# Optimization experiments

Hardware: AMD Instinct MI355X
Metric: run time of the kernel (lower is better)

## Reference

```python
import jax, jax.numpy as jnp
import numpy as np

B, IN_DIM, OUT_DIM = 4096, 2048, 2048
EMA_M = 0.95
LN_EPS = 1e-5


def setup_inputs() -> dict:
    key = jax.random.key(0)
    ks = jax.random.split(key, 8)
    x = jax.random.normal(ks[0], (B, IN_DIM), dtype=jnp.float32)
    # W_slow is orthogonal-init in torch (gain 0.5); scaled gaussian is a fine stand-in for math testing
    W_slow = jax.random.normal(ks[1], (OUT_DIM, IN_DIM), dtype=jnp.float32) * (0.5 / np.sqrt(IN_DIM))
    # buffers start at zero in torch; use small nonzero values so the medium/fast GEMMs are exercised
    W_medium = jax.random.normal(ks[2], (OUT_DIM, IN_DIM), dtype=jnp.float32) * 0.01
    W_fast = jax.random.normal(ks[3], (OUT_DIM, IN_DIM), dtype=jnp.float32) * 0.01
    ln_gamma = jnp.ones((OUT_DIM,), jnp.float32) + 0.1 * jax.random.normal(ks[4], (OUT_DIM,), dtype=jnp.float32)
    ln_beta = 0.1 * jax.random.normal(ks[5], (OUT_DIM,), dtype=jnp.float32)
    pc_w1 = jax.random.normal(ks[6], (8, 3), dtype=jnp.float32) * 0.5
    pc_b1 = jnp.zeros((8,), jnp.float32)
    pc_w2 = jax.random.normal(ks[7], (1, 8), dtype=jnp.float32) * 0.5
    pc_b2 = jnp.full((1,), -1.5, jnp.float32)  # torch fills last Linear bias with -1.5
    ema_mean = jnp.zeros((1,), jnp.float32)
    ema_std = jnp.ones((1,), jnp.float32)
    return {"x": x, "W_slow": W_slow, "W_medium": W_medium, "W_fast": W_fast,
            "ln_gamma": ln_gamma, "ln_beta": ln_beta,
            "pc_w1": pc_w1, "pc_b1": pc_b1, "pc_w2": pc_w2, "pc_b2": pc_b2,
            "ema_mean": ema_mean, "ema_std": ema_std}


def reference(x, W_slow, W_medium, W_fast, ln_gamma, ln_beta,
              pc_w1, pc_b1, pc_w2, pc_b2, ema_mean, ema_std):
    xc = jnp.clip(x, -5.0, 5.0)
    slow_out = jnp.clip(xc @ W_slow.T, -10.0, 10.0)
    pre_act = jnp.clip(slow_out + xc @ W_medium.T + xc @ W_fast.T, -10.0, 10.0)  # [B, OUT]

    batch_mean = pre_act.mean(axis=1, keepdims=True)                      # [B,1]
    batch_std = jnp.maximum(pre_act.std(axis=1, keepdims=True), 1e-6)     # [B,1], ddof=0

    # EMA buffer update (no-grad in torch); clamps applied after update
    new_mean = jnp.clip(EMA_M * ema_mean + (1.0 - EMA_M) * batch_mean.mean(), -0.5, 0.5)
    new_std = jnp.clip(EMA_M * ema_std + (1.0 - EMA_M) * batch_std.mean(), 0.1, 1.5)
    homeostasis = new_std / (jnp.abs(new_mean) + 1e-6)                    # [1]

    stats = jnp.concatenate([batch_mean, batch_std,
                             jnp.broadcast_to(homeostasis[None, :], (batch_mean.shape[0], 1))], axis=1)  # [B,3]
    h = jax.nn.gelu(stats @ pc_w1.T + pc_b1, approximate=False)           # torch GELU is exact erf
    learned_plasticity = jax.nn.sigmoid(h @ pc_w2.T + pc_b2)[:, 0]        # [B] (does not affect `out`)
    _ = learned_plasticity  # kept for fidelity with original compute graph

    # LayerNorm over last dim, eps=1e-5
    mu = pre_act.mean(axis=-1, keepdims=True)
    var = pre_act.var(axis=-1, keepdims=True)
    normed = (pre_act - mu) * jax.lax.rsqrt(var + LN_EPS) * ln_gamma + ln_beta
    out = 5.0 * jnp.tanh(normed / 5.0)
    return out
```

## Files before the change

### kernel.cpp

```cpp
#include <hip/hip_runtime.h>
#include <hip/hip_bf16.h>

#define BDIM    4096
#define IN_DIM  2048
#define OUT_DIM 2048

typedef __attribute__((ext_vector_type(4))) float  floatx4;
typedef __attribute__((ext_vector_type(8))) short  bf16x8;

__device__ __forceinline__ unsigned short f2bf(float f) {
    union { float f; unsigned u; } v; v.f = f;
    unsigned r = v.u + 0x7FFFu + ((v.u >> 16) & 1u);
    return (unsigned short)(r >> 16);
}

__device__ __forceinline__ float bf2f(unsigned short h) {
    union { unsigned u; float f; } v; v.u = (unsigned)h << 16;
    return v.f;
}

__device__ __forceinline__ void async16(const unsigned short* g, unsigned short* l) {
    __builtin_amdgcn_global_load_lds(
        (const __attribute__((address_space(1))) unsigned int*)g,
        (__attribute__((address_space(3))) unsigned int*)l,
        16, 0, 0);
}

__global__ __launch_bounds__(256) void prep(const float* __restrict__ x,
                                            const float* __restrict__ Ws,
                                            const float* __restrict__ Wm,
                                            const float* __restrict__ Wf,
                                            unsigned short* __restrict__ xc,
                                            unsigned short* __restrict__ bsum) {
    int b = blockIdx.x;
    if (b < 8192) {
        int i = b * 256 + threadIdx.x;
        float4 v = ((const float4*)x)[i];
        ushort4 o;
        o.x = f2bf(fminf(fmaxf(v.x, -5.f), 5.f));
        o.y = f2bf(fminf(fmaxf(v.y, -5.f), 5.f));
        o.z = f2bf(fminf(fmaxf(v.z, -5.f), 5.f));
        o.w = f2bf(fminf(fmaxf(v.w, -5.f), 5.f));
        ((ushort4*)xc)[i] = o;
    } else {
        int i = (b - 8192) * 256 + threadIdx.x;
        float4 s = ((const float4*)Ws)[i];
        float4 m = ((const float4*)Wm)[i];
        float4 f = ((const float4*)Wf)[i];
        ushort4 o;
        o.x = f2bf(s.x + m.x + f.x);
        o.y = f2bf(s.y + m.y + f.y);
        o.z = f2bf(s.z + m.z + f.z);
        o.w = f2bf(s.w + m.w + f.w);
        ((ushort4*)bsum)[i] = o;
    }
}

#define TILE   128
#define BK     64
#define KSPLIT 2
#define KHALF  (IN_DIM / KSPLIT)
#define ITERS  (KHALF / BK)

#define MEMBAR() asm volatile("" ::: "memory")

__global__ __launch_bounds__(256, 3) void gemm_bt(const unsigned short* __restrict__ A,
                                                  const unsigned short* __restrict__ B,
                                                  unsigned short* __restrict__ Cpart) {
    constexpr int N = OUT_DIM, K = IN_DIM;
    __shared__ __align__(16) unsigned short As[2 * TILE * BK];
    __shared__ __align__(16) unsigned short Bs[TILE * BK];

    const int tid  = threadIdx.x;
    const int lane = tid & 63;
    const int wave = tid >> 6;
    const int wm   = (wave >> 1) * 64;
    const int wn   = (wave & 1) * 64;
    const int rowBlock = blockIdx.y * TILE;
    const int colBlock = blockIdx.x * TILE;
    const int kBase    = blockIdx.z * KHALF;
    unsigned short* C = Cpart + (size_t)blockIdx.z * BDIM * OUT_DIM;

    const int sRow = tid >> 3;
    const int sSeg = (tid & 7) ^ (sRow & 7);
    const unsigned short* aSrc = A + (size_t)(rowBlock + sRow) * K + kBase + sSeg * 8;
    const unsigned short* bSrc = B + (size_t)(colBlock + sRow) * K + kBase + sSeg * 8;

    floatx4 acc[4][4] = {};

    const int fragRow = lane & 15;
    const int quad    = lane >> 4;
    const int l7      = lane & 7;

    auto stageA = [&](int t, int p) {
        unsigned short* ad = As + p * TILE * BK + tid * 8;
        const unsigned short* ag = aSrc + t * BK;
#pragma unroll
        for (int r = 0; r < 4; r++)
            async16(ag + (size_t)(r * 32) * K, ad + r * 32 * BK);
    };
    auto stageB = [&](int t) {
        unsigned short* bd = Bs + tid * 8;
        const unsigned short* bg = bSrc + t * BK;
#pragma unroll
        for (int r = 0; r < 4; r++)
            async16(bg + (size_t)(r * 32) * K, bd + r * 32 * BK);
    };

    stageB(0);
    stageA(0, 0);
    stageA(1, 1);
    __builtin_amdgcn_s_waitcnt(0xF74);
    MEMBAR();
    __builtin_amdgcn_s_barrier();
    MEMBAR();

    for (int k = 0; k < ITERS; k++) {
        const unsigned short* Ab = As + (k & 1) * TILE * BK;

#pragma unroll
        for (int kk = 0; kk < 2; kk++) {
            const int xs = ((quad + kk * 4) ^ l7) << 3;
            bf16x8 af[4], bfr[4];
#pragma unroll
            for (int i = 0; i < 4; i++) {
                af[i]  = *(const bf16x8*)(Ab + (wm + i * 16 + fragRow) * BK + xs);
                bfr[i] = *(const bf16x8*)(Bs + (wn + i * 16 + fragRow) * BK + xs);
            }
#pragma unroll
            for (int i = 0; i < 4; i++)
#pragma unroll
                for (int j = 0; j < 4; j++)
                    acc[i][j] = __builtin_amdgcn_mfma_f32_16x16x32_bf16(af[i], bfr[j], acc[i][j], 0, 0, 0);
        }

        if (k == ITERS - 1) break;
        MEMBAR();
        __builtin_amdgcn_s_barrier();
        MEMBAR();
        stageB(k + 1);
        if (k + 2 < ITERS) {
            stageA(k + 2, k & 1);
            __builtin_amdgcn_s_waitcnt(0xF74);
        } else {
            __builtin_amdgcn_s_waitcnt(0xF70);
        }
        MEMBAR();
        __builtin_amdgcn_s_barrier();
        MEMBAR();
    }

    const int cCol = colBlock + wn + (lane & 15);
    const int cRow = rowBlock + wm + quad * 4;
#pragma unroll
    for (int i = 0; i < 4; i++) {
#pragma unroll
        for (int j = 0; j < 4; j++) {
            const int col = cCol + j * 16;
            const int rb  = cRow + i * 16;
#pragma unroll
            for (int r = 0; r < 4; r++)
                C[(size_t)(rb + r) * N + col] = f2bf(acc[i][j][r]);
        }
    }
}

__global__ __launch_bounds__(256) void ln_kernel(const unsigned short* __restrict__ Cpart,
                                                 const float* __restrict__ gamma,
                                                 const float* __restrict__ beta,
                                                 float* __restrict__ out) {
    const int row = blockIdx.x;
    const int tid = threadIdx.x;
    __shared__ float wsum[4], wsq[4];

    const uint2* Ca = (const uint2*)(Cpart + (size_t)row * OUT_DIM);
    const uint2* Cb = (const uint2*)(Cpart + (size_t)BDIM * OUT_DIM + (size_t)row * OUT_DIM);

    float4 p[2];
    float sum = 0.f, sq = 0.f;
#pragma unroll
    for (int it = 0; it < 2; it++) {
        uint2 ua = Ca[tid + it * 256];
        uint2 ub = Cb[tid + it * 256];
        float4 q;
        q.x = bf2f((unsigned short)(ua.x & 0xFFFF)) + bf2f((unsigned short)(ub.x & 0xFFFF));
        q.y = bf2f((unsigned short)(ua.x >> 16))    + bf2f((unsigned short)(ub.x >> 16));
        q.z = bf2f((unsigned short)(ua.y & 0xFFFF)) + bf2f((unsigned short)(ub.y & 0xFFFF));
        q.w = bf2f((unsigned short)(ua.y >> 16))    + bf2f((unsigned short)(ub.y >> 16));
        q.x = fminf(fmaxf(q.x, -10.f), 10.f);
        q.y = fminf(fmaxf(q.y, -10.f), 10.f);
        q.z = fminf(fmaxf(q.z, -10.f), 10.f);
        q.w = fminf(fmaxf(q.w, -10.f), 10.f);
        p[it] = q;
        sum += q.x + q.y + q.z + q.w;
        sq  += q.x * q.x + q.y * q.y + q.z * q.z + q.w * q.w;
    }
#pragma unroll
    for (int off = 32; off > 0; off >>= 1) {
        sum += __shfl_down(sum, off);
        sq  += __shfl_down(sq,  off);
    }
    if ((tid & 63) == 0) { wsum[tid >> 6] = sum; wsq[tid >> 6] = sq; }
    __syncthreads();
    const float tsum = wsum[0] + wsum[1] + wsum[2] + wsum[3];
    const float tsq  = wsq[0]  + wsq[1]  + wsq[2]  + wsq[3];
    const float mu   = tsum * (1.0f / OUT_DIM);
    const float var  = tsq * (1.0f / OUT_DIM) - mu * mu;
    const float inv  = rsqrtf(var + 1e-5f);

#pragma unroll
    for (int it = 0; it < 2; it++) {
        int i = tid + it * 256;
        float4 q = p[it];
        float4 g = *(const float4*)(gamma + i * 4);
        float4 b = *(const float4*)(beta + i * 4);
        float4 o;
        float zx = (q.x - mu) * inv * g.x + b.x;
        float zy = (q.y - mu) * inv * g.y + b.y;
        float zz = (q.z - mu) * inv * g.z + b.z;
        float zw = (q.w - mu) * inv * g.w + b.w;
        o.x = 5.f * (1.f - 2.f / (__expf(0.4f * zx) + 1.f));
        o.y = 5.f * (1.f - 2.f / (__expf(0.4f * zy) + 1.f));
        o.z = 5.f * (1.f - 2.f / (__expf(0.4f * zz) + 1.f));
        o.w = 5.f * (1.f - 2.f / (__expf(0.4f * zw) + 1.f));
        *(float4*)(out + (size_t)row * OUT_DIM + i * 4) = o;
    }
}

extern "C" void kernel_launch(void* const* d_in, const int* in_sizes, int n_in,
                              void* d_out, int out_size, void* d_ws, size_t ws_size,
                              hipStream_t stream) {
    const float* x     = (const float*)d_in[0];
    const float* Ws    = (const float*)d_in[1];
    const float* Wm    = (const float*)d_in[2];
    const float* Wf    = (const float*)d_in[3];
    const float* gamma = (const float*)d_in[4];
    const float* beta  = (const float*)d_in[5];
    float* out = (float*)d_out;

    char* ws = (char*)d_ws;
    unsigned short* xc   = (unsigned short*)ws;
    unsigned short* bsum = (unsigned short*)(ws + (size_t)16 * 1024 * 1024);
    unsigned short* Cbuf = (unsigned short*)(ws + (size_t)24 * 1024 * 1024);

    prep<<<12288, 256, 0, stream>>>(x, Ws, Wm, Wf, xc, bsum);
    dim3 g(OUT_DIM / TILE, BDIM / TILE, KSPLIT);
    gemm_bt<<<g, 256, 0, stream>>>(xc, bsum, Cbuf);
    ln_kernel<<<BDIM, 256, 0, stream>>>(Cbuf, gamma, beta, out);
}
```

Baseline: 185.3 us.

## Load B fragments directly from global into registers, drop B LDS staging

Removes the shared-memory staging buffer for the B (weight) tile. Each wave now loads its MFMA B fragments straight from global memory into registers, double-buffered across the two k-halves and prefetched one iteration ahead. This cuts LDS footprint and LDS read/write traffic, which may allow higher occupancy. In exchange each wave issues redundant, less coalesced global loads (16-byte chunks strided across rows), and the waitcnt values are retuned to match the new count of outstanding loads.

```diff
diff --git a/kernel.cpp b/kernel.cpp
--- a/kernel.cpp
+++ b/kernel.cpp
@@ -69,7 +69,6 @@
                                                   unsigned short* __restrict__ Cpart) {
     constexpr int N = OUT_DIM, K = IN_DIM;
     __shared__ __align__(16) unsigned short As[2 * TILE * BK];
-    __shared__ __align__(16) unsigned short Bs[TILE * BK];
 
     const int tid  = threadIdx.x;
     const int lane = tid & 63;
@@ -84,7 +83,6 @@
     const int sRow = tid >> 3;
     const int sSeg = (tid & 7) ^ (sRow & 7);
     const unsigned short* aSrc = A + (size_t)(rowBlock + sRow) * K + kBase + sSeg * 8;
-    const unsigned short* bSrc = B + (size_t)(colBlock + sRow) * K + kBase + sSeg * 8;
 
     floatx4 acc[4][4] = {};
 
@@ -92,6 +90,11 @@
     const int quad    = lane >> 4;
     const int l7      = lane & 7;
 
+    const unsigned short* bF0 = B + (size_t)(colBlock + wn +  0 + fragRow) * K + kBase + quad * 8;
+    const unsigned short* bF1 = B + (size_t)(colBlock + wn + 16 + fragRow) * K + kBase + quad * 8;
+    const unsigned short* bF2 = B + (size_t)(colBlock + wn + 32 + fragRow) * K + kBase + quad * 8;
+    const unsigned short* bF3 = B + (size_t)(colBlock + wn + 48 + fragRow) * K + kBase + quad * 8;
+
     auto stageA = [&](int t, int p) {
         unsigned short* ad = As + p * TILE * BK + tid * 8;
         const unsigned short* ag = aSrc + t * BK;
@@ -99,51 +102,66 @@
         for (int r = 0; r < 4; r++)
             async16(ag + (size_t)(r * 32) * K, ad + r * 32 * BK);
     };
-    auto stageB = [&](int t) {
-        unsigned short* bd = Bs + tid * 8;
-        const unsigned short* bg = bSrc + t * BK;
-#pragma unroll
-        for (int r = 0; r < 4; r++)
-            async16(bg + (size_t)(r * 32) * K, bd + r * 32 * BK);
-    };
-
-    stageB(0);
+
+    bf16x8 b0[4], b1[4];
+
     stageA(0, 0);
     stageA(1, 1);
-    __builtin_amdgcn_s_waitcnt(0xF74);
+    MEMBAR();
+    b0[0] = *(const bf16x8*)(bF0); b0[1] = *(const bf16x8*)(bF1);
+    b0[2] = *(const bf16x8*)(bF2); b0[3] = *(const bf16x8*)(bF3);
+    b1[0] = *(const bf16x8*)(bF0 + 32); b1[1] = *(const bf16x8*)(bF1 + 32);
+    b1[2] = *(const bf16x8*)(bF2 + 32); b1[3] = *(const bf16x8*)(bF3 + 32);
+    MEMBAR();
+    __builtin_amdgcn_s_waitcnt(0x0F7C);
     MEMBAR();
     __builtin_amdgcn_s_barrier();
     MEMBAR();
 
     for (int k = 0; k < ITERS; k++) {
         const unsigned short* Ab = As + (k & 1) * TILE * BK;
-
-#pragma unroll
-        for (int kk = 0; kk < 2; kk++) {
-            const int xs = ((quad + kk * 4) ^ l7) << 3;
-            bf16x8 af[4], bfr[4];
-#pragma unroll
-            for (int i = 0; i < 4; i++) {
-                af[i]  = *(const bf16x8*)(Ab + (wm + i * 16 + fragRow) * BK + xs);
-                bfr[i] = *(const bf16x8*)(Bs + (wn + i * 16 + fragRow) * BK + xs);
-            }
+        int sn = 2 * (k + 1); if (sn >= 2 * ITERS) sn = 0;
+        const int off0 = sn * 32, off1 = off0 + 32;
+
+        {
+            const int xs = (quad ^ l7) << 3;
+            bf16x8 af[4];
+#pragma unroll
+            for (int i = 0; i < 4; i++)
+                af[i] = *(const bf16x8*)(Ab + (wm + i * 16 + fragRow) * BK + xs);
 #pragma unroll
             for (int i = 0; i < 4; i++)
 #pragma unroll
                 for (int j = 0; j < 4; j++)
-                    acc[i][j] = __builtin_amdgcn_mfma_f32_16x16x32_bf16(af[i], bfr[j], acc[i][j], 0, 0, 0);
-        }
+                    acc[i][j] = __builtin_amdgcn_mfma_f32_16x16x32_bf16(af[i], b0[j], acc[i][j], 0, 0, 0);
+        }
+        b0[0] = *(const bf16x8*)(bF0 + off0); b0[1] = *(const bf16x8*)(bF1 + off0);
+        b0[2] = *(const bf16x8*)(bF2 + off0); b0[3] = *(const bf16x8*)(bF3 + off0);
+
+        {
+            const int xs = ((quad + 4) ^ l7) << 3;
+            bf16x8 af[4];
+#pragma unroll
+            for (int i = 0; i < 4; i++)
+                af[i] = *(const bf16x8*)(Ab + (wm + i * 16 + fragRow) * BK + xs);
+#pragma unroll
+            for (int i = 0; i < 4; i++)
+#pragma unroll
+                for (int j = 0; j < 4; j++)
+                    acc[i][j] = __builtin_amdgcn_mfma_f32_16x16x32_bf16(af[i], b1[j], acc[i][j], 0, 0, 0);
+        }
+        b1[0] = *(const bf16x8*)(bF0 + off1); b1[1] = *(const bf16x8*)(bF1 + off1);
+        b1[2] = *(const bf16x8*)(bF2 + off1); b1[3] = *(const bf16x8*)(bF3 + off1);
 
         if (k == ITERS - 1) break;
         MEMBAR();
         __builtin_amdgcn_s_barrier();
         MEMBAR();
-        stageB(k + 1);
         if (k + 2 < ITERS) {
             stageA(k + 2, k & 1);
-            __builtin_amdgcn_s_waitcnt(0xF74);
+            __builtin_amdgcn_s_waitcnt(0x0F7C);
         } else {
-            __builtin_amdgcn_s_waitcnt(0xF70);
+            __builtin_amdgcn_s_waitcnt(0x0F78);
         }
         MEMBAR();
         __builtin_amdgcn_s_barrier();
```

Result: slower. 219.3 us (+18.4%).
